# Kernel tuning notes

Hardware: AMD Instinct MI355X
Metric: run time of the kernel (lower is better)

The kernel has to match this reference:

```python
import jax, jax.numpy as jnp
import numpy as np

B, N, A = 8, 256, 180  # batch, resolution (even), n_angles


def setup_inputs() -> dict:
    key = jax.random.key(0)
    imgs = jax.random.normal(jax.random.fold_in(key, 0), (B, N, N), dtype=jnp.float32)
    # uniformly spaced projection angles over [0, pi)
    angles = jnp.linspace(0.0, np.pi, A, endpoint=False).astype(jnp.float32)
    return {"imgs": imgs, "angles": angles}


def _radon_forward(imgs, angles):
    """Parallel-beam Radon forward projection via bilinear ray sampling.

    imgs:   [B, N, N] float image batch
    angles: [A] float projection angles (radians)
    returns sinogram [B, A, N] (detector count == resolution, unit step along ray)
    """
    n = imgs.shape[-1]
    dtype = imgs.dtype
    c = (n - 1) / 2.0  # image center in pixel coords
    s = jnp.arange(n, dtype=dtype) - c  # detector positions, centered
    t = s                                # integration steps along each ray
    cos = jnp.cos(angles)[:, None, None]  # [A,1,1]
    sin = jnp.sin(angles)[:, None, None]
    # Sample point for (angle a, detector s_i, step t_j), in pixel coordinates.
    x = s[None, :, None] * cos - t[None, None, :] * sin + c  # [A, N, N]
    y = s[None, :, None] * sin + t[None, None, :] * cos + c  # [A, N, N]

    x0 = jnp.floor(x)
    y0 = jnp.floor(y)
    wx = x - x0
    wy = y - y0
    x0i = x0.astype(jnp.int32)
    y0i = y0.astype(jnp.int32)

    def corner(xi, yi, w):
        # zero-padding outside the image: mask out-of-range samples
        inb = (xi >= 0) & (xi < n) & (yi >= 0) & (yi < n)
        xc = jnp.clip(xi, 0, n - 1)
        yc = jnp.clip(yi, 0, n - 1)
        vals = imgs[:, yc, xc]  # gather -> [B, A, N, N]
        return vals * (w * inb.astype(dtype))[None]

    acc = (corner(x0i, y0i, (1.0 - wx) * (1.0 - wy))
           + corner(x0i + 1, y0i, wx * (1.0 - wy))
           + corner(x0i, y0i + 1, (1.0 - wx) * wy)
           + corner(x0i + 1, y0i + 1, wx * wy))
    return acc.sum(axis=-1)  # line integral along t -> [B, A, N]


def reference(imgs, angles):
    return _radon_forward(imgs, angles)
```

## Files before the change

### kernel.cpp

```cpp
#include <hip/hip_runtime.h>
#include <hip/hip_fp16.h>

#define NREZ 256
#define NB 8
#define NA 180

#define GW 258
#define GBYTES ((size_t)GW * GW * 16)

#define LW 72
#define LH 46
#define QTAB 0x64317520u
#define CHUNK_T 32
#define NCHUNK (NREZ / CHUNK_T)

__device__ __forceinline__ __half2 bc_h2(unsigned int v) {
    return __builtin_bit_cast(__half2, v);
}

__device__ __forceinline__ void dma16(const uint4* g, uint4* l) {
    __builtin_amdgcn_global_load_lds(
        (const __attribute__((address_space(1))) void*)g,
        (__attribute__((address_space(3))) void*)l, 16, 0, 0);
}

__global__ __launch_bounds__(256) void build_fp16g(const float* __restrict__ img,
                                                   uint4* __restrict__ gbuf) {
    const int p = blockIdx.x * 256 + threadIdx.x;
    const int y = p >> 8, x = p & 255;
    unsigned short h[NB];
#pragma unroll
    for (int b = 0; b < NB; ++b)
        h[b] = __half_as_ushort(__float2half_rn(img[b * (NREZ * NREZ) + p]));
    uint4 v;
    v.x = (unsigned)h[0] | ((unsigned)h[1] << 16);
    v.y = (unsigned)h[2] | ((unsigned)h[3] << 16);
    v.z = (unsigned)h[4] | ((unsigned)h[5] << 16);
    v.w = (unsigned)h[6] | ((unsigned)h[7] << 16);
    gbuf[(size_t)(y + 1) * GW + (x + 1)] = v;
}

__global__ __launch_bounds__(256) void radon_dma(const uint4* __restrict__ gbuf,
                                                 const float* __restrict__ angles,
                                                 float* __restrict__ out) {
    __shared__ uint4 tile[LW * LH];

    const int a = blockIdx.x;
    const int tid = threadIdx.x;
    const int wave = tid >> 6;
    const int lane = tid & 63;
    const int s_sub = lane & 7;
    const int t_sub = lane >> 3;
    const int sIdx = blockIdx.y * 32 + wave * 8 + s_sub;

    const float C = 127.5f;
    float sn, cs;
    sincosf(angles[a], &sn, &cs);
    const float s = (float)sIdx - C;
    const float xs = fmaf(s, cs, C);
    const float ys = fmaf(s, sn, C);

    const float s_lo = (float)(blockIdx.y * 32) - C;
    const float s_hi = s_lo + 31.f;
    const float xsl = fmaf(s_lo, cs, C), xsh = fmaf(s_hi, cs, C);
    const float ysl = fmaf(s_lo, sn, C), ysh = fmaf(s_hi, sn, C);

    auto window = [&](int ck, int& bxs, int& bys) {
        const float t_lo = (float)(ck * CHUNK_T) - C;
        const float t_hi = t_lo + 31.f;
        const float x00 = fmaf(t_lo, -sn, xsl), x01 = fmaf(t_hi, -sn, xsl);
        const float x10 = fmaf(t_lo, -sn, xsh), x11 = fmaf(t_hi, -sn, xsh);
        const float y00 = fmaf(t_lo, cs, ysl), y01 = fmaf(t_hi, cs, ysl);
        const float y10 = fmaf(t_lo, cs, ysh), y11 = fmaf(t_hi, cs, ysh);
        const int bx = (int)floorf(fminf(fminf(x00, x01), fminf(x10, x11)));
        const int by = (int)floorf(fminf(fminf(y00, y01), fminf(y10, y11)));
        bxs = min(max(bx, -1), 193);
        bys = min(max(by, -1), 212);
    };

    auto stage = [&](int bxs, int bys) {
#pragma unroll
        for (int k = 0; k < 12; ++k) {
            const int row = wave + 4 * k;
            if (row < LH) {
                const int gy = bys + row;
                if (gy <= 256) {
                    const unsigned qr = (QTAB >> ((row & 7) << 2)) & 7u;
                    const uint4* gp = gbuf + (size_t)(gy + 1) * GW + (bxs + 1) + lane;
                    dma16(gp, &tile[row * LW + qr]);
                }
            }
        }
    };

    float accf[NB];
#pragma unroll
    for (int b = 0; b < NB; ++b) accf[b] = 0.f;
    const __half2 hz = __float2half2_rn(0.f);

    int bxs, bys;
    window(0, bxs, bys);
    stage(bxs, bys);

    for (int ck = 0; ck < NCHUNK; ++ck) {
        __syncthreads();

        const float t_lo = (float)(ck * CHUNK_T) - C;
        __half2 acc01 = hz, acc23 = hz, acc45 = hz, acc67 = hz;
#pragma unroll
        for (int it = 0; it < 4; ++it) {
            const float tt = t_lo + (float)(t_sub + 8 * it);
            const float x = fmaf(tt, -sn, xs);
            const float y = fmaf(tt, cs, ys);
            const float xf = floorf(x), yf = floorf(y);
            const int u0 = (int)xf, v0 = (int)yf;
            if (u0 >= -1 && u0 <= 255 && v0 >= -1 && v0 <= 255) {
                const float wu = x - xf, wv = y - yf;
                const float au = 1.f - wu, av = 1.f - wv;
                const __half2 w00 = __float2half2_rn(au * av);
                const __half2 w10 = __float2half2_rn(wu * av);
                const __half2 w01 = __float2half2_rn(au * wv);
                const __half2 w11 = __float2half2_rn(wu * wv);
                const int dx = u0 - bxs;
                const int r = v0 - bys;
                const unsigned qr0 = (QTAB >> ((r & 7) << 2)) & 7u;
                const unsigned qr1 = (QTAB >> (((r + 1) & 7) << 2)) & 7u;
                const int b00 = r * LW + (int)qr0 + dx;
                const int b10 = (r + 1) * LW + (int)qr1 + dx;
                const uint4 p00 = tile[b00];
                const uint4 p10 = tile[b00 + 1];
                const uint4 p01 = tile[b10];
                const uint4 p11 = tile[b10 + 1];
                acc01 = __hfma2(w00, bc_h2(p00.x), acc01);
                acc01 = __hfma2(w10, bc_h2(p10.x), acc01);
                acc01 = __hfma2(w01, bc_h2(p01.x), acc01);
                acc01 = __hfma2(w11, bc_h2(p11.x), acc01);
                acc23 = __hfma2(w00, bc_h2(p00.y), acc23);
                acc23 = __hfma2(w10, bc_h2(p10.y), acc23);
                acc23 = __hfma2(w01, bc_h2(p01.y), acc23);
                acc23 = __hfma2(w11, bc_h2(p11.y), acc23);
                acc45 = __hfma2(w00, bc_h2(p00.z), acc45);
                acc45 = __hfma2(w10, bc_h2(p10.z), acc45);
                acc45 = __hfma2(w01, bc_h2(p01.z), acc45);
                acc45 = __hfma2(w11, bc_h2(p11.z), acc45);
                acc67 = __hfma2(w00, bc_h2(p00.w), acc67);
                acc67 = __hfma2(w10, bc_h2(p10.w), acc67);
                acc67 = __hfma2(w01, bc_h2(p01.w), acc67);
                acc67 = __hfma2(w11, bc_h2(p11.w), acc67);
            }
        }
        accf[0] += __low2float(acc01); accf[1] += __high2float(acc01);
        accf[2] += __low2float(acc23); accf[3] += __high2float(acc23);
        accf[4] += __low2float(acc45); accf[5] += __high2float(acc45);
        accf[6] += __low2float(acc67); accf[7] += __high2float(acc67);

        __syncthreads();

        if (ck + 1 < NCHUNK) {
            window(ck + 1, bxs, bys);
            stage(bxs, bys);
        }
    }

#pragma unroll
    for (int b = 0; b < NB; ++b) {
        float v = accf[b];
        v += __shfl_xor(v, 8);
        v += __shfl_xor(v, 16);
        v += __shfl_xor(v, 32);
        accf[b] = v;
    }
    if (t_sub == 0) {
#pragma unroll
        for (int b = 0; b < NB; ++b) {
            out[(b * NA + a) * NREZ + sIdx] = accf[b];
        }
    }
}

__global__ __launch_bounds__(256) void radon_plain(const float* __restrict__ img,
                                                   const float* __restrict__ angles,
                                                   float* __restrict__ out) {
    const int a = blockIdx.x;
    const int tid = threadIdx.x;
    const int wave = tid >> 6;
    const int lane = tid & 63;
    const int s_sub = lane & 7;
    const int t_sub = lane >> 3;
    const int sIdx = blockIdx.y * 32 + wave * 8 + s_sub;
    const float c = 127.5f;
    float sn, cs;
    sincosf(angles[a], &sn, &cs);
    const float s = (float)sIdx - c;
    float acc[NB];
#pragma unroll
    for (int b = 0; b < NB; ++b) acc[b] = 0.f;
    for (int j = 0; j < NREZ / 8; ++j) {
        const float tt = (float)(t_sub + 8 * j) - c;
        const float x = s * cs - tt * sn + c;
        const float y = s * sn + tt * cs + c;
        const float xf = floorf(x), yf = floorf(y);
        const int u0 = (int)xf, v0 = (int)yf;
        if (u0 < -1 || u0 >= NREZ || v0 < -1 || v0 >= NREZ) continue;
        const float wu = x - xf, wv = y - yf;
        const bool iu0 = (u0 >= 0), iu1 = (u0 + 1 <= NREZ - 1);
        const bool iv0 = (v0 >= 0), iv1 = (v0 + 1 <= NREZ - 1);
        const float w00 = (1.f - wu) * (1.f - wv) * ((iu0 && iv0) ? 1.f : 0.f);
        const float w10 = wu * (1.f - wv) * ((iu1 && iv0) ? 1.f : 0.f);
        const float w01 = (1.f - wu) * wv * ((iu0 && iv1) ? 1.f : 0.f);
        const float w11 = wu * wv * ((iu1 && iv1) ? 1.f : 0.f);
        const int u0c = min(max(u0, 0), NREZ - 1);
        const int u1c = min(u0 + 1, NREZ - 1);
        const int v0c = min(max(v0, 0), NREZ - 1);
        const int v1c = min(v0 + 1, NREZ - 1);
#pragma unroll
        for (int b = 0; b < NB; ++b) {
            const float* p = img + b * (NREZ * NREZ);
            acc[b] += w00 * p[v0c * NREZ + u0c] + w10 * p[v0c * NREZ + u1c] +
                      w01 * p[v1c * NREZ + u0c] + w11 * p[v1c * NREZ + u1c];
        }
    }
#pragma unroll
    for (int b = 0; b < NB; ++b) {
        float v = acc[b];
        v += __shfl_xor(v, 8);
        v += __shfl_xor(v, 16);
        v += __shfl_xor(v, 32);
        acc[b] = v;
    }
    if (t_sub == 0) {
#pragma unroll
        for (int b = 0; b < NB; ++b) out[(b * NA + a) * NREZ + sIdx] = acc[b];
    }
}

extern "C" void kernel_launch(void* const* d_in, const int* in_sizes, int n_in,
                              void* d_out, int out_size, void* d_ws, size_t ws_size,
                              hipStream_t stream) {
    (void)in_sizes; (void)n_in; (void)out_size;
    const float* imgs = (const float*)d_in[0];
    const float* angles = (const float*)d_in[1];
    float* out = (float*)d_out;

    dim3 grid(NA, NREZ / 32);
    if (ws_size >= GBYTES) {
        uint4* gbuf = (uint4*)d_ws;
        hipMemsetAsync(gbuf, 0, GBYTES, stream);
        build_fp16g<<<NREZ * NREZ / 256, 256, 0, stream>>>(imgs, gbuf);
        radon_dma<<<grid, 256, 0, stream>>>(gbuf, angles, out);
    } else {
        radon_plain<<<grid, 256, 0, stream>>>(imgs, angles, out);
    }
}
```

Before: 95.41 us.

## Fold padding into build kernel, skip bounds checks and narrow DMA rows

Removes the separate memset by having the fp16 packing kernel write the zero border itself. The radon kernel now marks chunks whose sampling window lies fully inside the image and runs an unchecked sampling loop for them. It also limits the DMA staging to 48 lanes per row when the window is not clamped, and looks up both swizzle offsets with one packed 64-bit table. The aim is to cut a launch, branch work and LDS traffic. The cost is a duplicated sampling loop and more bounds-reasoning complexity.

Measured after the change: 94.31 us. About the same (-1.1%).

```diff
diff --git a/kernel.cpp b/kernel.cpp
--- a/kernel.cpp
+++ b/kernel.cpp
@@ -11,6 +11,7 @@
 #define LW 72
 #define LH 46
 #define QTAB 0x64317520u
+#define QPTAB 0x0664433117755220ull
 #define CHUNK_T 32
 #define NCHUNK (NREZ / CHUNK_T)
 
@@ -26,18 +27,23 @@
 
 __global__ __launch_bounds__(256) void build_fp16g(const float* __restrict__ img,
                                                    uint4* __restrict__ gbuf) {
-    const int p = blockIdx.x * 256 + threadIdx.x;
-    const int y = p >> 8, x = p & 255;
-    unsigned short h[NB];
-#pragma unroll
-    for (int b = 0; b < NB; ++b)
-        h[b] = __half_as_ushort(__float2half_rn(img[b * (NREZ * NREZ) + p]));
-    uint4 v;
-    v.x = (unsigned)h[0] | ((unsigned)h[1] << 16);
-    v.y = (unsigned)h[2] | ((unsigned)h[3] << 16);
-    v.z = (unsigned)h[4] | ((unsigned)h[5] << 16);
-    v.w = (unsigned)h[6] | ((unsigned)h[7] << 16);
-    gbuf[(size_t)(y + 1) * GW + (x + 1)] = v;
+    const int gy = blockIdx.x;
+    for (int gx = threadIdx.x; gx < GW; gx += 256) {
+        uint4 v = make_uint4(0u, 0u, 0u, 0u);
+        const int x = gx - 1, y = gy - 1;
+        if (x >= 0 && x < NREZ && y >= 0 && y < NREZ) {
+            const int p = (y << 8) + x;
+            unsigned short h[NB];
+#pragma unroll
+            for (int b = 0; b < NB; ++b)
+                h[b] = __half_as_ushort(__float2half_rn(img[b * (NREZ * NREZ) + p]));
+            v.x = (unsigned)h[0] | ((unsigned)h[1] << 16);
+            v.y = (unsigned)h[2] | ((unsigned)h[3] << 16);
+            v.z = (unsigned)h[4] | ((unsigned)h[5] << 16);
+            v.w = (unsigned)h[6] | ((unsigned)h[7] << 16);
+        }
+        gbuf[(size_t)gy * GW + gx] = v;
+    }
 }
 
 __global__ __launch_bounds__(256) void radon_dma(const uint4* __restrict__ gbuf,
@@ -65,7 +71,7 @@
     const float xsl = fmaf(s_lo, cs, C), xsh = fmaf(s_hi, cs, C);
     const float ysl = fmaf(s_lo, sn, C), ysh = fmaf(s_hi, sn, C);
 
-    auto window = [&](int ck, int& bxs, int& bys) {
+    auto window = [&](int ck, int& bxs, int& bys, bool& interior, int& wl) {
         const float t_lo = (float)(ck * CHUNK_T) - C;
         const float t_hi = t_lo + 31.f;
         const float x00 = fmaf(t_lo, -sn, xsl), x01 = fmaf(t_hi, -sn, xsl);
@@ -76,15 +82,17 @@
         const int by = (int)floorf(fminf(fminf(y00, y01), fminf(y10, y11)));
         bxs = min(max(bx, -1), 193);
         bys = min(max(by, -1), 212);
+        interior = (bx >= 0) && (by >= 0) && (bx + 46 <= 255) && (by + 46 <= 255);
+        wl = (bx >= -1 && bx <= 193) ? 48 : 64;
     };
 
-    auto stage = [&](int bxs, int bys) {
+    auto stage = [&](int bxs, int bys, int wl) {
 #pragma unroll
         for (int k = 0; k < 12; ++k) {
             const int row = wave + 4 * k;
             if (row < LH) {
                 const int gy = bys + row;
-                if (gy <= 256) {
+                if (gy <= 256 && lane < wl) {
                     const unsigned qr = (QTAB >> ((row & 7) << 2)) & 7u;
                     const uint4* gp = gbuf + (size_t)(gy + 1) * GW + (bxs + 1) + lane;
                     dma16(gp, &tile[row * LW + qr]);
@@ -98,23 +106,23 @@
     for (int b = 0; b < NB; ++b) accf[b] = 0.f;
     const __half2 hz = __float2half2_rn(0.f);
 
-    int bxs, bys;
-    window(0, bxs, bys);
-    stage(bxs, bys);
+    int bxs, bys, wl;
+    bool interior;
+    window(0, bxs, bys, interior, wl);
+    stage(bxs, bys, wl);
 
     for (int ck = 0; ck < NCHUNK; ++ck) {
         __syncthreads();
 
         const float t_lo = (float)(ck * CHUNK_T) - C;
         __half2 acc01 = hz, acc23 = hz, acc45 = hz, acc67 = hz;
-#pragma unroll
-        for (int it = 0; it < 4; ++it) {
-            const float tt = t_lo + (float)(t_sub + 8 * it);
+
+        auto samp = [&](float tt, bool chk) {
             const float x = fmaf(tt, -sn, xs);
             const float y = fmaf(tt, cs, ys);
             const float xf = floorf(x), yf = floorf(y);
             const int u0 = (int)xf, v0 = (int)yf;
-            if (u0 >= -1 && u0 <= 255 && v0 >= -1 && v0 <= 255) {
+            if (!chk || (u0 >= -1 && u0 <= 255 && v0 >= -1 && v0 <= 255)) {
                 const float wu = x - xf, wv = y - yf;
                 const float au = 1.f - wu, av = 1.f - wv;
                 const __half2 w00 = __float2half2_rn(au * av);
@@ -123,10 +131,9 @@
                 const __half2 w11 = __float2half2_rn(wu * wv);
                 const int dx = u0 - bxs;
                 const int r = v0 - bys;
-                const unsigned qr0 = (QTAB >> ((r & 7) << 2)) & 7u;
-                const unsigned qr1 = (QTAB >> (((r + 1) & 7) << 2)) & 7u;
-                const int b00 = r * LW + (int)qr0 + dx;
-                const int b10 = (r + 1) * LW + (int)qr1 + dx;
+                const unsigned pp = (unsigned)(QPTAB >> ((r & 7) << 3));
+                const int b00 = r * LW + (int)(pp & 7u) + dx;
+                const int b10 = (r + 1) * LW + (int)((pp >> 4) & 7u) + dx;
                 const uint4 p00 = tile[b00];
                 const uint4 p10 = tile[b00 + 1];
                 const uint4 p01 = tile[b10];
@@ -148,7 +155,18 @@
                 acc67 = __hfma2(w01, bc_h2(p01.w), acc67);
                 acc67 = __hfma2(w11, bc_h2(p11.w), acc67);
             }
-        }
+        };
+
+        if (interior) {
+#pragma unroll
+            for (int it = 0; it < 4; ++it)
+                samp(t_lo + (float)(t_sub + 8 * it), false);
+        } else {
+#pragma unroll
+            for (int it = 0; it < 4; ++it)
+                samp(t_lo + (float)(t_sub + 8 * it), true);
+        }
+
         accf[0] += __low2float(acc01); accf[1] += __high2float(acc01);
         accf[2] += __low2float(acc23); accf[3] += __high2float(acc23);
         accf[4] += __low2float(acc45); accf[5] += __high2float(acc45);
@@ -157,8 +175,8 @@
         __syncthreads();
 
         if (ck + 1 < NCHUNK) {
-            window(ck + 1, bxs, bys);
-            stage(bxs, bys);
+            window(ck + 1, bxs, bys, interior, wl);
+            stage(bxs, bys, wl);
         }
     }
 
@@ -245,8 +263,7 @@
     dim3 grid(NA, NREZ / 32);
     if (ws_size >= GBYTES) {
         uint4* gbuf = (uint4*)d_ws;
-        hipMemsetAsync(gbuf, 0, GBYTES, stream);
-        build_fp16g<<<NREZ * NREZ / 256, 256, 0, stream>>>(imgs, gbuf);
+        build_fp16g<<<GW, 256, 0, stream>>>(imgs, gbuf);
         radon_dma<<<grid, 256, 0, stream>>>(gbuf, angles, out);
     } else {
         radon_plain<<<grid, 256, 0, stream>>>(imgs, angles, out);
```
